# Kernel optimization log

Hardware: AMD Instinct MI355X
Metric: run time of the kernel (lower is better)

## Reference

```python
import jax, jax.numpy as jnp
import numpy as np

B, N, L = 8, 170, 336
PATCH = 16
P = L // PATCH            # 21 patches, pad_len = 0
D_MODEL = 128
D_STATE = 16
D_CONV = 4
D_INNER = 2 * D_MODEL     # expand=2
DT_RANK = 8               # ceil(d_model/16)
PRED_LEN = 96


def setup_inputs() -> dict:
    key = jax.random.key(0)
    ks = jax.random.split(key, 16)
    def nrm(k, shape, s=0.02):
        return jax.random.normal(k, shape, jnp.float32) * s
    return {
        "x": jax.random.normal(ks[0], (B, N, L), jnp.float32),
        "node_embed_map": nrm(ks[1], (1, N, 1, D_MODEL)),
        "pe_W": nrm(ks[2], (D_MODEL, PATCH), 0.1),
        "pe_b": jnp.zeros((D_MODEL,), jnp.float32),
        "pos_emb": nrm(ks[3], (1, 1, P, D_MODEL)),
        "r_W1": nrm(ks[4], (D_MODEL // 4, 3), 0.3),
        "r_b1": jnp.zeros((D_MODEL // 4,), jnp.float32),
        "r_W2": nrm(ks[5], (D_MODEL, D_MODEL // 4), 0.1),
        "r_b2": jnp.zeros((D_MODEL,), jnp.float32),
        "ln_g": jnp.ones((D_MODEL,), jnp.float32),
        "ln_b": jnp.zeros((D_MODEL,), jnp.float32),
        "in_proj_W": nrm(ks[6], (2 * D_INNER, D_MODEL), 0.05),
        "conv_W": nrm(ks[7], (D_INNER, D_CONV), 0.2),
        "conv_b": jnp.zeros((D_INNER,), jnp.float32),
        "x_proj_W": nrm(ks[8], (DT_RANK + 2 * D_STATE, D_INNER), 0.05),
        "dt_proj_W": nrm(ks[9], (D_INNER, DT_RANK), 0.3),
        "dt_proj_b": nrm(ks[10], (D_INNER,), 0.5),
        "A_log": jnp.log(jnp.broadcast_to(jnp.arange(1.0, D_STATE + 1.0, dtype=jnp.float32), (D_INNER, D_STATE))),
        "D_skip": jnp.ones((D_INNER,), jnp.float32),
        "out_proj_W": nrm(ks[11], (D_MODEL, D_INNER), 0.05),
        "head_W": nrm(ks[12], (PRED_LEN, P * D_MODEL), 0.02),
        "head_b": jnp.zeros((PRED_LEN,), jnp.float32),
    }


def _layernorm(x, g, b, eps=1e-5):
    mu = x.mean(-1, keepdims=True)
    var = ((x - mu) ** 2).mean(-1, keepdims=True)
    return (x - mu) * jax.lax.rsqrt(var + eps) * g + b


def _router(x_patch, r_W1, r_b1, r_W2, r_b2):
    # FFT energy over each length-16 patch -> low/mid/high band features -> tiny MLP gate
    X = jnp.fft.rfft(x_patch, axis=-1)          # [M, P, 9]
    energy = X.real ** 2 + X.imag ** 2
    fl = energy.shape[-1]
    s1, s2 = fl // 3, 2 * fl // 3
    feats = jnp.stack([energy[..., :s1].sum(-1),
                       energy[..., s1:s2].sum(-1),
                       energy[..., s2:].sum(-1)], axis=-1)
    feats = feats / (feats.sum(-1, keepdims=True) + 1e-6)
    h = jax.nn.relu(feats @ r_W1.T + r_b1)
    return jax.nn.sigmoid(h @ r_W2.T + r_b2)    # [M, P, d_model]


def _mamba(u, in_proj_W, conv_W, conv_b, x_proj_W, dt_proj_W, dt_proj_b, A_log, D_skip, out_proj_W):
    # u: [M, T, d_model]  (Mamba block: in_proj -> causal dwconv -> SSM scan -> gate -> out_proj)
    M, T, _ = u.shape
    xz = u @ in_proj_W.T                        # [M, T, 2*d_inner]
    xc, z = jnp.split(xz, 2, axis=-1)
    # causal depthwise conv1d, kernel D_CONV
    xp = jnp.pad(xc, ((0, 0), (D_CONV - 1, 0), (0, 0)))
    conv = conv_b + sum(xp[:, k:k + T, :] * conv_W[:, k] for k in range(D_CONV))
    xs = jax.nn.silu(conv)                      # [M, T, d_inner]
    proj = xs @ x_proj_W.T                      # [M, T, dt_rank + 2*d_state]
    dt_in = proj[..., :DT_RANK]
    Bm = proj[..., DT_RANK:DT_RANK + D_STATE]
    Cm = proj[..., DT_RANK + D_STATE:]
    dt = jax.nn.softplus(dt_in @ dt_proj_W.T + dt_proj_b)  # [M, T, d_inner]
    A = -jnp.exp(A_log)                         # [d_inner, d_state]

    def step(h, inp):
        dt_t, B_t, C_t, u_t = inp               # [M,d_inner], [M,d_state], [M,d_state], [M,d_inner]
        dA = jnp.exp(dt_t[..., None] * A)       # [M, d_inner, d_state]
        h = dA * h + (dt_t * u_t)[..., None] * B_t[:, None, :]
        y = jnp.einsum('mds,ms->md', h, C_t)
        return h, y

    h0 = jnp.zeros((M, D_INNER, D_STATE), jnp.float32)
    _, ys = jax.lax.scan(step, h0, (jnp.moveaxis(dt, 1, 0), jnp.moveaxis(Bm, 1, 0),
                                    jnp.moveaxis(Cm, 1, 0), jnp.moveaxis(xs, 1, 0)))
    y = jnp.moveaxis(ys, 0, 1) + xs * D_skip
    y = y * jax.nn.silu(z)
    return y @ out_proj_W.T


def reference(x, node_embed_map, pe_W, pe_b, pos_emb, r_W1, r_b1, r_W2, r_b2,
              ln_g, ln_b, in_proj_W, conv_W, conv_b, x_proj_W, dt_proj_W, dt_proj_b,
              A_log, D_skip, out_proj_W, head_W, head_b):
    Bb, Nn, _ = x.shape
    x_patches = x.reshape(Bb, Nn, P, PATCH)                     # pad_len == 0 for L=336
    x_enc = x_patches @ pe_W.T + pe_b + pos_emb + node_embed_map
    x_enc_flat = x_enc.reshape(Bb * Nn, P, D_MODEL)
    gate = _router(x_patches.reshape(Bb * Nn, P, PATCH), r_W1, r_b1, r_W2, r_b2)
    x_gated = _layernorm(x_enc_flat, ln_g, ln_b) * gate
    y = _mamba(x_gated, in_proj_W, conv_W, conv_b, x_proj_W, dt_proj_W, dt_proj_b,
               A_log, D_skip, out_proj_W)
    out = (y + x_enc_flat).reshape(Bb, Nn, P * D_MODEL)         # dropout is identity (eval)
    return out @ head_W.T + head_b                              # [B, N, pred_len]
```

## Files before the change

### kernel.cpp

```cpp
#include <hip/hip_runtime.h>
#include <math.h>

#define B_ 8
#define N_ 170
#define L_ 336
#define PATCH_ 16
#define P_ 21
#define DM_ 128
#define DS_ 16
#define DI_ 256
#define PL_ 96
#define M_ (B_ * N_)
#define T_ 21
#define R_ (M_ * T_)
#define KF_ (P_ * DM_)

#define XST 260
#define ZST 256
#define UST2 130
#define EST 128

typedef __attribute__((ext_vector_type(8))) short short8;
typedef __attribute__((ext_vector_type(4))) float f32x4;
typedef __attribute__((ext_vector_type(2))) float f32x2;

__device__ inline unsigned short f2b(float f) {
    unsigned int u = __builtin_bit_cast(unsigned int, f);
    u += 0x7fff + ((u >> 16) & 1);
    return (unsigned short)(u >> 16);
}
__device__ inline float b2f(unsigned short h) {
    unsigned int u = ((unsigned int)h) << 16;
    return __builtin_bit_cast(float, u);
}
__device__ inline float fast_sigmoid(float v) {
    return __builtin_amdgcn_rcpf(1.f + __expf(-v));
}
__device__ inline f32x2 pk_fma(f32x2 a, f32x2 b, f32x2 c) {
    f32x2 d;
    asm("v_pk_fma_f32 %0, %1, %2, %3" : "=v"(d) : "v"(a), "v"(b), "v"(c));
    return d;
}
__device__ inline f32x2 pk_mul(f32x2 a, f32x2 b) {
    f32x2 d;
    asm("v_pk_mul_f32 %0, %1, %2" : "=v"(d) : "v"(a), "v"(b));
    return d;
}
__device__ inline f32x2 pk_add(f32x2 a, f32x2 b) {
    f32x2 d;
    asm("v_pk_add_f32 %0, %1, %2" : "=v"(d) : "v"(a), "v"(b));
    return d;
}
__device__ inline unsigned int cvt_pk_bf16(float a, float b) {
    unsigned int d;
    asm("v_cvt_pk_bf16_f32 %0, %1, %2" : "=v"(d) : "v"(a), "v"(b));
    return d;
}

__global__ __launch_bounds__(256) void k_convert(
    const float* __restrict__ inW, const float* __restrict__ xpW,
    const float* __restrict__ outW, const float* __restrict__ hW,
    const float* __restrict__ peW, const float* __restrict__ rW2,
    unsigned short* __restrict__ winb, unsigned short* __restrict__ wxpb,
    unsigned short* __restrict__ woutb, unsigned short* __restrict__ whb,
    unsigned short* __restrict__ peWb, unsigned short* __restrict__ rW2b)
{
    const int base = (blockIdx.x * 256 + threadIdx.x) * 2;
#pragma unroll
    for (int u = 0; u < 2; ++u) {
        int i = base + u;
        if (i < 65536) { winb[i] = f2b(inW[i]); continue; }
        i -= 65536;
        if (i < 16384) {
            int j = i >> 8;
            wxpb[i] = (j < 40) ? f2b(xpW[j * 256 + (i & 255)]) : (unsigned short)0;
            continue;
        }
        i -= 16384;
        if (i < 32768) { woutb[i] = f2b(outW[i]); continue; }
        i -= 32768;
        if (i < 258048) { whb[i] = f2b(hW[i]); continue; }
        i -= 258048;
        if (i < 4096) {
            int r = i >> 5, j = i & 31;
            peWb[i] = (j < 16) ? f2b(peW[r * 16 + j]) : (unsigned short)0;
            continue;
        }
        i -= 4096;
        if (i < 4096) { rW2b[i] = f2b(rW2[i]); }
    }
}

__global__ __launch_bounds__(256, 4) void k_fused(
    const float* __restrict__ x, const float* __restrict__ nem,
    const unsigned short* __restrict__ peWb, const float* __restrict__ peB,
    const float* __restrict__ posE,
    const float* __restrict__ rW1, const float* __restrict__ rB1,
    const unsigned short* __restrict__ rW2b, const float* __restrict__ rB2,
    const float* __restrict__ lnG, const float* __restrict__ lnB,
    const unsigned short* __restrict__ winb,
    const float* __restrict__ convW, const float* __restrict__ convB,
    const unsigned short* __restrict__ wxpb,
    const float* __restrict__ dtW, const float* __restrict__ dtB,
    const float* __restrict__ Dsk,
    const unsigned short* __restrict__ woutb,
    unsigned short* __restrict__ feat)
{
    __shared__ __align__(16) char lds[27136];
    unsigned short* xss   = (unsigned short*)(lds + 0);
    unsigned short* zsl   = (unsigned short*)(lds + 10920);
    unsigned short* usj   = (unsigned short*)(lds + 21672);
    float*          pjs   = (float*)(lds + 21680);
    unsigned short* gs    = (unsigned short*)(lds + 0);
    unsigned short* pa    = (unsigned short*)(lds + 8192);
    float*          es    = (float*)(lds + 10920);
    float*          ctst  = (float*)(lds + 11680);
    float*          pn    = (float*)(lds + 11808);
    unsigned short* xencs = (unsigned short*)(lds + 12320);
    unsigned short* ha    = (unsigned short*)(lds + 21680);

    const int m = blockIdx.x;
    const int n = m % N_;
    const int tid = threadIdx.x;
    const int lane = tid & 63;
    const int w = tid >> 6;
    const int lo = lane & 15, kq = (lane >> 4) * 8;
    const int rl = (lane >> 4) * 4, cl = lane & 15;

    unsigned int resp[2][2][2];

    if (tid < 84) {
        const float4 f = *(const float4*)(x + m * L_ + tid * 4);
        const int p = tid >> 2, jj = (tid & 3) * 4;
        unsigned int u0 = cvt_pk_bf16(f.x, f.y);
        unsigned int u1 = cvt_pk_bf16(f.z, f.w);
        *(uint2*)&pa[p * 40 + jj] = make_uint2(u0, u1);
    }
    for (int i = tid; i < 384; i += 256) {
        const int p = i / 12, q = i - p * 12;
        *(unsigned int*)&pa[p * 40 + 16 + q * 2] = 0u;
    }
    if (tid < 88) {
        const int p = 21 + tid / 8, q = tid & 7;
        *(unsigned int*)&pa[p * 40 + q * 2] = 0u;
    }
    if (tid < 16) {
        float s, c;
        sincosf((float)tid * (6.283185307179586f / 16.f), &s, &c);
        ctst[tid] = c; ctst[16 + tid] = s;
    }
    if (tid >= 64 && tid < 192) pn[tid - 64] = peB[tid - 64] + nem[n * DM_ + tid - 64];
    __syncthreads();

    if (tid < P_ * 9) {
        const int i = tid;
        const int p = i / 9, bin = i - p * 9;
        short8 xv0 = *(const short8*)&pa[p * 40];
        short8 xv1 = *(const short8*)&pa[p * 40 + 8];
        float re = 0.f, im = 0.f;
#pragma unroll
        for (int j = 0; j < PATCH_; ++j) {
            int idx = (bin * j) & 15;
            float xv = b2f((unsigned short)((j < 8) ? xv0[j] : xv1[j - 8]));
            re = fmaf(xv, ctst[idx], re);
            im = fmaf(xv, -ctst[16 + idx], im);
        }
        es[i] = re * re + im * im;
    }
    {
        const unsigned short* bb = peWb + (w * 32 + lo) * 32 + kq;
        short8 b0 = *(const short8*)bb;
        short8 b1 = *(const short8*)(bb + 16 * 32);
        short8 a0 = *(const short8*)&pa[lo * 40 + kq];
        short8 a1 = *(const short8*)&pa[(16 + lo) * 40 + kq];
        f32x4 z = {0.f, 0.f, 0.f, 0.f};
        f32x4 C[2][2];
        C[0][0] = __builtin_amdgcn_mfma_f32_16x16x32_bf16(a0, b0, z, 0, 0, 0);
        C[0][1] = __builtin_amdgcn_mfma_f32_16x16x32_bf16(a0, b1, z, 0, 0, 0);
        C[1][0] = __builtin_amdgcn_mfma_f32_16x16x32_bf16(a1, b0, z, 0, 0, 0);
        C[1][1] = __builtin_amdgcn_mfma_f32_16x16x32_bf16(a1, b1, z, 0, 0, 0);
#pragma unroll
        for (int mi = 0; mi < 2; ++mi)
#pragma unroll
            for (int ni = 0; ni < 2; ++ni) {
                const int col = w * 32 + ni * 16 + cl;
                const float pncol = pn[col];
                const int row0 = mi * 16 + rl;
                const int rc0 = (row0 + 0 < P_) ? row0 + 0 : P_ - 1;
                const int rc1 = (row0 + 1 < P_) ? row0 + 1 : P_ - 1;
                const int rc2 = (row0 + 2 < P_) ? row0 + 2 : P_ - 1;
                const int rc3 = (row0 + 3 < P_) ? row0 + 3 : P_ - 1;
                float v0 = C[mi][ni][0] + pncol + posE[rc0 * DM_ + col];
                float v1 = C[mi][ni][1] + pncol + posE[rc1 * DM_ + col];
                float v2 = C[mi][ni][2] + pncol + posE[rc2 * DM_ + col];
                float v3 = C[mi][ni][3] + pncol + posE[rc3 * DM_ + col];
                const unsigned int p0 = cvt_pk_bf16(v0, v1);
                const unsigned int p1 = cvt_pk_bf16(v2, v3);
                resp[mi][ni][0] = p0;
                resp[mi][ni][1] = p1;
                xencs[(row0 + 0) * EST + col] = (unsigned short)p0;
                xencs[(row0 + 1) * EST + col] = (unsigned short)(p0 >> 16);
                xencs[(row0 + 2) * EST + col] = (unsigned short)p1;
                xencs[(row0 + 3) * EST + col] = (unsigned short)(p1 >> 16);
            }
    }
    __syncthreads();

    for (int idx = tid; idx < P_ * 32; idx += 256) {
        const int p = idx >> 5, i = idx & 31;
        const float* e = &es[p * 9];
        float b0 = e[0] + e[1] + e[2];
        float b1 = e[3] + e[4] + e[5];
        float b2 = e[6] + e[7] + e[8];
        float inv = __builtin_amdgcn_rcpf(b0 + b1 + b2 + 1e-6f);
        float hv = rB1[i];
        hv = fmaf(b0 * inv, rW1[i * 3 + 0], hv);
        hv = fmaf(b1 * inv, rW1[i * 3 + 1], hv);
        hv = fmaf(b2 * inv, rW1[i * 3 + 2], hv);
        ha[p * 40 + i] = f2b(hv > 0.f ? hv : 0.f);
    }
    __syncthreads();

    {
        const unsigned short* bb = rW2b + (w * 32 + lo) * 32 + kq;
        short8 b0 = *(const short8*)bb;
        short8 b1 = *(const short8*)(bb + 16 * 32);
        short8 a0 = *(const short8*)&ha[lo * 40 + kq];
        short8 a1 = *(const short8*)&ha[(16 + lo) * 40 + kq];
        f32x4 z = {0.f, 0.f, 0.f, 0.f};
        f32x4 C[2][2];
        C[0][0] = __builtin_amdgcn_mfma_f32_16x16x32_bf16(a0, b0, z, 0, 0, 0);
        C[0][1] = __builtin_amdgcn_mfma_f32_16x16x32_bf16(a0, b1, z, 0, 0, 0);
        C[1][0] = __builtin_amdgcn_mfma_f32_16x16x32_bf16(a1, b0, z, 0, 0, 0);
        C[1][1] = __builtin_amdgcn_mfma_f32_16x16x32_bf16(a1, b1, z, 0, 0, 0);
#pragma unroll
        for (int mi = 0; mi < 2; ++mi)
#pragma unroll
            for (int ni = 0; ni < 2; ++ni) {
                const int col = w * 32 + ni * 16 + cl;
                const float rb = rB2[col];
                float s0 = fast_sigmoid(C[mi][ni][0] + rb);
                float s1 = fast_sigmoid(C[mi][ni][1] + rb);
                float s2 = fast_sigmoid(C[mi][ni][2] + rb);
                float s3 = fast_sigmoid(C[mi][ni][3] + rb);
                const unsigned int p0 = cvt_pk_bf16(s0, s1);
                const unsigned int p1 = cvt_pk_bf16(s2, s3);
                const int row0 = mi * 16 + rl;
                gs[(row0 + 0) * EST + col] = (unsigned short)p0;
                gs[(row0 + 1) * EST + col] = (unsigned short)(p0 >> 16);
                gs[(row0 + 2) * EST + col] = (unsigned short)p1;
                gs[(row0 + 3) * EST + col] = (unsigned short)(p1 >> 16);
            }
    }
    __syncthreads();

    {
        const float lg0 = lnG[lane], lg1 = lnG[lane + 64];
        const float lb0 = lnB[lane], lb1 = lnB[lane + 64];
        for (int it = 0; it < 6; ++it) {
            const int p = it * 4 + w;
            if (p >= P_) continue;
            float xe0 = b2f(xencs[p * EST + lane]);
            float xe1 = b2f(xencs[p * EST + 64 + lane]);
            float g0 = b2f(gs[p * EST + lane]);
            float g1 = b2f(gs[p * EST + 64 + lane]);
            float s = xe0 + xe1, s2 = xe0 * xe0 + xe1 * xe1;
#pragma unroll
            for (int off = 32; off; off >>= 1) {
                s += __shfl_xor(s, off);
                s2 += __shfl_xor(s2, off);
            }
            float mu = s * (1.f / 128.f);
            float var = s2 * (1.f / 128.f) - mu * mu;
            float rs = rsqrtf(var + 1e-5f);
            float u0 = ((xe0 - mu) * rs * lg0 + lb0) * g0;
            float u1 = ((xe1 - mu) * rs * lg1 + lb1) * g1;
            const unsigned int pk = cvt_pk_bf16(u0, u1);
            usj[p * UST2 + lane]      = (unsigned short)pk;
            usj[p * UST2 + 64 + lane] = (unsigned short)(pk >> 16);
        }
    }
    __syncthreads();

    {
        const int rA1 = (16 + lo > P_ - 1) ? (P_ - 1) : (16 + lo);
#pragma unroll 1
        for (int pp = 0; pp < 4; ++pp) {
            f32x4 C[2][2];
#pragma unroll
            for (int mi = 0; mi < 2; ++mi)
#pragma unroll
                for (int ni = 0; ni < 2; ++ni) C[mi][ni] = (f32x4){0.f, 0.f, 0.f, 0.f};

            const unsigned short* bbase = winb + (size_t)(w * 128 + pp * 32 + lo) * DM_ + kq;
            __builtin_amdgcn_s_setprio(1);
#pragma unroll
            for (int k0 = 0; k0 < DM_; k0 += 32) {
                short8 a0 = *(const short8*)&usj[lo * UST2 + k0 + kq];
                short8 a1 = *(const short8*)&usj[rA1 * UST2 + k0 + kq];
#pragma unroll
                for (int ni = 0; ni < 2; ++ni) {
                    short8 b = *(const short8*)(bbase + ni * 16 * DM_ + k0);
                    C[0][ni] = __builtin_amdgcn_mfma_f32_16x16x32_bf16(a0, b, C[0][ni], 0, 0, 0);
                    C[1][ni] = __builtin_amdgcn_mfma_f32_16x16x32_bf16(a1, b, C[1][ni], 0, 0, 0);
                }
            }
            __builtin_amdgcn_s_setprio(0);
            const int cb0 = (w & 1) * 128 + pp * 32 + cl;
            if (w < 2) {
#pragma unroll
                for (int ni = 0; ni < 2; ++ni) {
                    const int col = cb0 + ni * 16;
#pragma unroll
                    for (int mi = 0; mi < 2; ++mi) {
                        const unsigned int p0 = cvt_pk_bf16(C[mi][ni][0], C[mi][ni][1]);
                        const unsigned int p1 = cvt_pk_bf16(C[mi][ni][2], C[mi][ni][3]);
                        const int row0 = mi * 16 + rl;
                        if (row0 + 0 < T_) xss[(row0 + 0) * XST + col] = (unsigned short)p0;
                        if (row0 + 1 < T_) xss[(row0 + 1) * XST + col] = (unsigned short)(p0 >> 16);
                        if (row0 + 2 < T_) xss[(row0 + 2) * XST + col] = (unsigned short)p1;
                        if (row0 + 3 < T_) xss[(row0 + 3) * XST + col] = (unsigned short)(p1 >> 16);
                    }
                }
            } else {
#pragma unroll
                for (int ni = 0; ni < 2; ++ni) {
                    const int col = cb0 + ni * 16;
#pragma unroll
                    for (int mi = 0; mi < 2; ++mi) {
                        float v0 = C[mi][ni][0]; v0 = v0 * fast_sigmoid(v0);
                        float v1 = C[mi][ni][1]; v1 = v1 * fast_sigmoid(v1);
                        float v2 = C[mi][ni][2]; v2 = v2 * fast_sigmoid(v2);
                        float v3 = C[mi][ni][3]; v3 = v3 * fast_sigmoid(v3);
                        const unsigned int p0 = cvt_pk_bf16(v0, v1);
                        const unsigned int p1 = cvt_pk_bf16(v2, v3);
                        const int row0 = mi * 16 + rl;
                        if (row0 + 0 < T_) zsl[(row0 + 0) * ZST + col] = (unsigned short)p0;
                        if (row0 + 1 < T_) zsl[(row0 + 1) * ZST + col] = (unsigned short)(p0 >> 16);
                        if (row0 + 2 < T_) zsl[(row0 + 2) * ZST + col] = (unsigned short)p1;
                        if (row0 + 3 < T_) zsl[(row0 + 3) * ZST + col] = (unsigned short)(p1 >> 16);
                    }
                }
            }
        }
    }
    __syncthreads();

    {
        const int d = tid;
        float4 cw = *(const float4*)(convW + d * 4);
        const float cb = convB[d];
        float c[T_];
#pragma unroll
        for (int t = 0; t < T_; ++t) c[t] = b2f(xss[t * XST + d]);
        float v[T_];
#pragma unroll
        for (int t = 0; t < T_; ++t) {
            float a0 = (t >= 3) ? c[t - 3] : 0.f;
            float a1 = (t >= 2) ? c[t - 2] : 0.f;
            float a2 = (t >= 1) ? c[t - 1] : 0.f;
            float vv = cb;
            vv = fmaf(a0, cw.x, vv);
            vv = fmaf(a1, cw.y, vv);
            vv = fmaf(a2, cw.z, vv);
            vv = fmaf(c[t], cw.w, vv);
            v[t] = vv * fast_sigmoid(vv);
        }
#pragma unroll
        for (int tp = 0; tp < 10; ++tp) {
            const unsigned int pk = cvt_pk_bf16(v[tp * 2], v[tp * 2 + 1]);
            xss[(tp * 2 + 0) * XST + d] = (unsigned short)pk;
            xss[(tp * 2 + 1) * XST + d] = (unsigned short)(pk >> 16);
        }
        xss[20 * XST + d] = (unsigned short)cvt_pk_bf16(v[20], v[20]);
    }
    __syncthreads();

    {
        const int mt = w >> 1, nt = w & 1;
        const unsigned short* ar = &xss[(mt * 16 + lo) * XST + kq];
        const unsigned short* bp0 = wxpb + (nt * 32 + lo) * DI_ + kq;
        const unsigned short* bp1 = bp0 + 16 * DI_;
        f32x4 c0 = {0.f, 0.f, 0.f, 0.f}, c1 = c0;
        __builtin_amdgcn_s_setprio(1);
#pragma unroll
        for (int k0 = 0; k0 < DI_; k0 += 32) {
            short8 a  = *(const short8*)(ar + k0);
            short8 b0 = *(const short8*)(bp0 + k0);
            short8 b1 = *(const short8*)(bp1 + k0);
            c0 = __builtin_amdgcn_mfma_f32_16x16x32_bf16(a, b0, c0, 0, 0, 0);
            c1 = __builtin_amdgcn_mfma_f32_16x16x32_bf16(a, b1, c1, 0, 0, 0);
        }
        __builtin_amdgcn_s_setprio(0);
#pragma unroll
        for (int r = 0; r < 4; ++r) {
            const int row = mt * 16 + rl + r;
            const int ca = nt * 32 + cl, cb = ca + 16;
            if (row < T_) {
                if (ca < 40) pjs[row * 40 + ca] = c0[r];
                if (cb < 40) pjs[row * 40 + cb] = c1[r];
            }
        }
    }
    __syncthreads();

    {
        const int d = tid;
        f32x2 dw2[4];
        {
            const f32x2* dtW2 = (const f32x2*)(dtW + d * 8);
#pragma unroll
            for (int q = 0; q < 4; ++q) dw2[q] = dtW2[q];
        }
        const float db = dtB[d], Dv = Dsk[d];
        const f32x4* pj4 = (const f32x4*)pjs;
        f32x2 h2[8];
#pragma unroll
        for (int q = 0; q < 8; ++q) h2[q] = (f32x2){0.f, 0.f};
        float ypend = 0.f;
#pragma unroll
        for (int t = 0; t < T_; ++t) {
            f32x4 d0 = pj4[t * 10 + 0];
            f32x4 d1 = pj4[t * 10 + 1];
            f32x2 acc = {db, 0.f};
            acc = pk_fma(__builtin_shufflevector(d0, d0, 0, 1), dw2[0], acc);
            acc = pk_fma(__builtin_shufflevector(d0, d0, 2, 3), dw2[1], acc);
            acc = pk_fma(__builtin_shufflevector(d1, d1, 0, 1), dw2[2], acc);
            acc = pk_fma(__builtin_shufflevector(d1, d1, 2, 3), dw2[3], acc);
            float a = acc.x + acc.y;
            float qe = __expf(a);
            float dt = (a > 20.f) ? a : __logf(1.f + qe);
            float e1 = __builtin_amdgcn_rcpf(1.f + qe);
            float e2 = e1 * e1;
            float ut = b2f(xss[t * XST + d]);
            float zq = b2f(zsl[t * ZST + d]);
            float wk = dt * ut;
            f32x2 wk2 = {wk, wk};
            f32x2 e22 = {e2, e2};
            f32x2 dA2 = {e1, e2};
            f32x2 y2 = {0.f, 0.f};
#pragma unroll
            for (int q2 = 0; q2 < 4; ++q2) {
                f32x4 B4 = pj4[t * 10 + 2 + q2];
                f32x4 C4 = pj4[t * 10 + 6 + q2];
#pragma unroll
                for (int hh = 0; hh < 2; ++hh) {
                    const int q = 2 * q2 + hh;
                    f32x2 Bq = hh ? __builtin_shufflevector(B4, B4, 2, 3)
                                  : __builtin_shufflevector(B4, B4, 0, 1);
                    f32x2 Cq = hh ? __builtin_shufflevector(C4, C4, 2, 3)
                                  : __builtin_shufflevector(C4, C4, 0, 1);
                    if (q) dA2 = pk_mul(dA2, e22);
                    h2[q] = pk_fma(dA2, h2[q], pk_mul(wk2, Bq));
                    y2 = pk_fma(h2[q], Cq, y2);
                }
            }
            float yv = fmaf(ut, Dv, y2.x + y2.y) * zq;
            if (t & 1) {
                const unsigned int pk = cvt_pk_bf16(ypend, yv);
                xss[(t - 1) * XST + d] = (unsigned short)pk;
                xss[t * XST + d]       = (unsigned short)(pk >> 16);
            } else {
                ypend = yv;
            }
        }
        xss[20 * XST + d] = (unsigned short)cvt_pk_bf16(ypend, ypend);
    }
    __syncthreads();

    {
        f32x4 C[2][2];
#pragma unroll
        for (int mi = 0; mi < 2; ++mi)
#pragma unroll
            for (int ni = 0; ni < 2; ++ni) C[mi][ni] = (f32x4){0.f, 0.f, 0.f, 0.f};

        const unsigned short* bbase = woutb + (size_t)(w * 32 + lo) * DI_ + kq;
        __builtin_amdgcn_s_setprio(1);
#pragma unroll
        for (int k0 = 0; k0 < DI_; k0 += 32) {
            short8 a0 = *(const short8*)&xss[lo * XST + k0 + kq];
            short8 a1 = *(const short8*)&xss[(16 + lo) * XST + k0 + kq];
#pragma unroll
            for (int ni = 0; ni < 2; ++ni) {
                short8 b = *(const short8*)(bbase + ni * 16 * DI_ + k0);
                C[0][ni] = __builtin_amdgcn_mfma_f32_16x16x32_bf16(a0, b, C[0][ni], 0, 0, 0);
                C[1][ni] = __builtin_amdgcn_mfma_f32_16x16x32_bf16(a1, b, C[1][ni], 0, 0, 0);
            }
        }
        __builtin_amdgcn_s_setprio(0);
        unsigned short* fb = feat + (size_t)m * T_ * DM_;
#pragma unroll
        for (int mi = 0; mi < 2; ++mi)
#pragma unroll
            for (int ni = 0; ni < 2; ++ni) {
                const int col = w * 32 + ni * 16 + cl;
                const unsigned int pr0 = resp[mi][ni][0];
                const unsigned int pr1 = resp[mi][ni][1];
                f32x2 r01, r23;
                r01.x = __builtin_bit_cast(float, pr0 << 16);
                r01.y = __builtin_bit_cast(float, pr0 & 0xffff0000u);
                r23.x = __builtin_bit_cast(float, pr1 << 16);
                r23.y = __builtin_bit_cast(float, pr1 & 0xffff0000u);
                f32x2 c01 = {C[mi][ni][0], C[mi][ni][1]};
                f32x2 c23 = {C[mi][ni][2], C[mi][ni][3]};
                f32x2 s01 = pk_add(c01, r01);
                f32x2 s23 = pk_add(c23, r23);
                const unsigned int q0 = cvt_pk_bf16(s01.x, s01.y);
                const unsigned int q1 = cvt_pk_bf16(s23.x, s23.y);
                const int row0 = mi * 16 + rl;
                if (row0 + 0 < T_) fb[(row0 + 0) * DM_ + col] = (unsigned short)q0;
                if (row0 + 1 < T_) fb[(row0 + 1) * DM_ + col] = (unsigned short)(q0 >> 16);
                if (row0 + 2 < T_) fb[(row0 + 2) * DM_ + col] = (unsigned short)q1;
                if (row0 + 3 < T_) fb[(row0 + 3) * DM_ + col] = (unsigned short)(q1 >> 16);
            }
    }
}

__global__ __launch_bounds__(512) void k_gemm_head(
    const unsigned short* __restrict__ feat, const unsigned short* __restrict__ W,
    const float* __restrict__ hB, float* __restrict__ out)
{
    __shared__ float red[8 * 512];
    const int bid = blockIdx.x;
    const int wm = bid / 3, wn = bid % 3;
    const int tid = threadIdx.x, w = tid >> 6, lane = tid & 63;
    const int r0 = wm * 16, n0 = wn * 32;
    const int lo = lane & 15, kq = (lane >> 4) * 8;
    const unsigned short* ap  = feat + (size_t)(r0 + lo) * KF_ + kq;
    const unsigned short* bp0 = W + (size_t)(n0 + lo) * KF_ + kq;
    const unsigned short* bp1 = bp0 + 16 * KF_;
    f32x4 c0 = {0.f, 0.f, 0.f, 0.f}, c1 = c0;
    for (int s = w; s < 84; s += 8) {
        const int k0 = s * 32;
        short8 a  = *(const short8*)(ap + k0);
        short8 b0 = *(const short8*)(bp0 + k0);
        short8 b1 = *(const short8*)(bp1 + k0);
        c0 = __builtin_amdgcn_mfma_f32_16x16x32_bf16(a, b0, c0, 0, 0, 0);
        c1 = __builtin_amdgcn_mfma_f32_16x16x32_bf16(a, b1, c1, 0, 0, 0);
    }
    float* rw = &red[w * 512 + lane * 8];
#pragma unroll
    for (int r = 0; r < 4; ++r) { rw[r] = c0[r]; rw[4 + r] = c1[r]; }
    __syncthreads();

    {
        const int f = tid;
        float s = red[f] + red[512 + f] + red[1024 + f] + red[1536 + f]
                + red[2048 + f] + red[2560 + f] + red[3072 + f] + red[3584 + f];
        const int l = f >> 3, v = f & 7;
        const int row = r0 + ((l >> 4) << 2) + (v & 3);
        const int col = n0 + (l & 15) + ((v >= 4) ? 16 : 0);
        out[row * PL_ + col] = s + hB[col];
    }
}

extern "C" void kernel_launch(void* const* d_in, const int* in_sizes, int n_in,
                              void* d_out, int out_size, void* d_ws, size_t ws_size,
                              hipStream_t stream)
{
    const float* x     = (const float*)d_in[0];
    const float* nem   = (const float*)d_in[1];
    const float* peW   = (const float*)d_in[2];
    const float* peB   = (const float*)d_in[3];
    const float* posE  = (const float*)d_in[4];
    const float* rW1   = (const float*)d_in[5];
    const float* rB1   = (const float*)d_in[6];
    const float* rW2   = (const float*)d_in[7];
    const float* rB2   = (const float*)d_in[8];
    const float* lnG   = (const float*)d_in[9];
    const float* lnB   = (const float*)d_in[10];
    const float* inW   = (const float*)d_in[11];
    const float* convW = (const float*)d_in[12];
    const float* convB = (const float*)d_in[13];
    const float* xpW   = (const float*)d_in[14];
    const float* dtW   = (const float*)d_in[15];
    const float* dtB   = (const float*)d_in[16];
    const float* Dsk   = (const float*)d_in[18];
    const float* outW  = (const float*)d_in[19];
    const float* hW    = (const float*)d_in[20];
    const float* hB    = (const float*)d_in[21];
    float* out = (float*)d_out;

    char* ws = (char*)d_ws;
    size_t off = 0;
    auto alloc = [&](size_t bytes) { size_t o = off; off = (off + bytes + 255) & ~(size_t)255; return o; };
    unsigned short* feat  = (unsigned short*)(ws + alloc((size_t)R_ * DM_ * 2));
    unsigned short* winb  = (unsigned short*)(ws + alloc(512 * 128 * 2));
    unsigned short* wxpb  = (unsigned short*)(ws + alloc(64 * 256 * 2));
    unsigned short* woutb = (unsigned short*)(ws + alloc(128 * 256 * 2));
    unsigned short* whb   = (unsigned short*)(ws + alloc(96 * KF_ * 2));
    unsigned short* peWb  = (unsigned short*)(ws + alloc(128 * 32 * 2));
    unsigned short* rW2b  = (unsigned short*)(ws + alloc(128 * 32 * 2));

    k_convert<<<744, 256, 0, stream>>>(inW, xpW, outW, hW, peW, rW2,
                                       winb, wxpb, woutb, whb, peWb, rW2b);
    k_fused<<<M_, 256, 0, stream>>>(x, nem, peWb, peB, posE,
                                    rW1, rB1, rW2b, rB2, lnG, lnB,
                                    winb, convW, convB, wxpb,
                                    dtW, dtB, Dsk, woutb, feat);
    k_gemm_head<<<255, 512, 0, stream>>>(feat, whb, hB, out);
}
```

Baseline: 182.2 us.

## Fuse head projection into fused Mamba kernel, removing feature round-trip

The separate head GEMM kernel is removed. Each fused block now keeps its 21x128 bf16 feature tile in LDS and computes the 96 outputs with scalar FMAs over a transposed, pair-packed head weight produced in the convert kernel. This drops the global write and re-read of the feature tensor and one kernel launch. In exchange, every block streams the full head weight (about 516 KB) through cache using non-MFMA scalar math on only 192 threads, which could cost more than it saves.

```diff
diff --git a/kernel.cpp b/kernel.cpp
--- a/kernel.cpp
+++ b/kernel.cpp
@@ -33,6 +33,12 @@
     unsigned int u = ((unsigned int)h) << 16;
     return __builtin_bit_cast(float, u);
 }
+__device__ inline float b2f_lo(unsigned int u) {
+    return __builtin_bit_cast(float, u << 16);
+}
+__device__ inline float b2f_hi(unsigned int u) {
+    return __builtin_bit_cast(float, u & 0xffff0000u);
+}
 __device__ inline float fast_sigmoid(float v) {
     return __builtin_amdgcn_rcpf(1.f + __expf(-v));
 }
@@ -62,7 +68,7 @@
     const float* __restrict__ outW, const float* __restrict__ hW,
     const float* __restrict__ peW, const float* __restrict__ rW2,
     unsigned short* __restrict__ winb, unsigned short* __restrict__ wxpb,
-    unsigned short* __restrict__ woutb, unsigned short* __restrict__ whb,
+    unsigned short* __restrict__ woutb, unsigned short* __restrict__ whbT,
     unsigned short* __restrict__ peWb, unsigned short* __restrict__ rW2b)
 {
     const int base = (blockIdx.x * 256 + threadIdx.x) * 2;
@@ -79,7 +85,12 @@
         i -= 16384;
         if (i < 32768) { woutb[i] = f2b(outW[i]); continue; }
         i -= 32768;
-        if (i < 258048) { whb[i] = f2b(hW[i]); continue; }
+        if (i < 258048) {
+            const int k2 = i / 192, r = i - k2 * 192;
+            const int c = r >> 1, p = r & 1;
+            whbT[i] = f2b(hW[c * KF_ + 2 * k2 + p]);
+            continue;
+        }
         i -= 258048;
         if (i < 4096) {
             int r = i >> 5, j = i & 31;
@@ -104,7 +115,8 @@
     const float* __restrict__ dtW, const float* __restrict__ dtB,
     const float* __restrict__ Dsk,
     const unsigned short* __restrict__ woutb,
-    unsigned short* __restrict__ feat)
+    const unsigned short* __restrict__ whbT, const float* __restrict__ hB,
+    float* __restrict__ out)
 {
     __shared__ __align__(16) char lds[27136];
     unsigned short* xss   = (unsigned short*)(lds + 0);
@@ -118,6 +130,8 @@
     float*          pn    = (float*)(lds + 11808);
     unsigned short* xencs = (unsigned short*)(lds + 12320);
     unsigned short* ha    = (unsigned short*)(lds + 21680);
+    unsigned short* fls   = (unsigned short*)(lds + 21680);
+    float*          redh  = (float*)(lds + 0);
 
     const int m = blockIdx.x;
     const int n = m % N_;
@@ -489,7 +503,6 @@
             }
         }
         __builtin_amdgcn_s_setprio(0);
-        unsigned short* fb = feat + (size_t)m * T_ * DM_;
 #pragma unroll
         for (int mi = 0; mi < 2; ++mi)
 #pragma unroll
@@ -509,49 +522,32 @@
                 const unsigned int q0 = cvt_pk_bf16(s01.x, s01.y);
                 const unsigned int q1 = cvt_pk_bf16(s23.x, s23.y);
                 const int row0 = mi * 16 + rl;
-                if (row0 + 0 < T_) fb[(row0 + 0) * DM_ + col] = (unsigned short)q0;
-                if (row0 + 1 < T_) fb[(row0 + 1) * DM_ + col] = (unsigned short)(q0 >> 16);
-                if (row0 + 2 < T_) fb[(row0 + 2) * DM_ + col] = (unsigned short)q1;
-                if (row0 + 3 < T_) fb[(row0 + 3) * DM_ + col] = (unsigned short)(q1 >> 16);
-            }
-    }
-}
-
-__global__ __launch_bounds__(512) void k_gemm_head(
-    const unsigned short* __restrict__ feat, const unsigned short* __restrict__ W,
-    const float* __restrict__ hB, float* __restrict__ out)
-{
-    __shared__ float red[8 * 512];
-    const int bid = blockIdx.x;
-    const int wm = bid / 3, wn = bid % 3;
-    const int tid = threadIdx.x, w = tid >> 6, lane = tid & 63;
-    const int r0 = wm * 16, n0 = wn * 32;
-    const int lo = lane & 15, kq = (lane >> 4) * 8;
-    const unsigned short* ap  = feat + (size_t)(r0 + lo) * KF_ + kq;
-    const unsigned short* bp0 = W + (size_t)(n0 + lo) * KF_ + kq;
-    const unsigned short* bp1 = bp0 + 16 * KF_;
-    f32x4 c0 = {0.f, 0.f, 0.f, 0.f}, c1 = c0;
-    for (int s = w; s < 84; s += 8) {
-        const int k0 = s * 32;
-        short8 a  = *(const short8*)(ap + k0);
-        short8 b0 = *(const short8*)(bp0 + k0);
-        short8 b1 = *(const short8*)(bp1 + k0);
-        c0 = __builtin_amdgcn_mfma_f32_16x16x32_bf16(a, b0, c0, 0, 0, 0);
-        c1 = __builtin_amdgcn_mfma_f32_16x16x32_bf16(a, b1, c1, 0, 0, 0);
-    }
-    float* rw = &red[w * 512 + lane * 8];
-#pragma unroll
-    for (int r = 0; r < 4; ++r) { rw[r] = c0[r]; rw[4 + r] = c1[r]; }
-    __syncthreads();
-
-    {
-        const int f = tid;
-        float s = red[f] + red[512 + f] + red[1024 + f] + red[1536 + f]
-                + red[2048 + f] + red[2560 + f] + red[3072 + f] + red[3584 + f];
-        const int l = f >> 3, v = f & 7;
-        const int row = r0 + ((l >> 4) << 2) + (v & 3);
-        const int col = n0 + (l & 15) + ((v >= 4) ? 16 : 0);
-        out[row * PL_ + col] = s + hB[col];
+                if (row0 + 0 < T_) fls[(row0 + 0) * DM_ + col] = (unsigned short)q0;
+                if (row0 + 1 < T_) fls[(row0 + 1) * DM_ + col] = (unsigned short)(q0 >> 16);
+                if (row0 + 2 < T_) fls[(row0 + 2) * DM_ + col] = (unsigned short)q1;
+                if (row0 + 3 < T_) fls[(row0 + 3) * DM_ + col] = (unsigned short)(q1 >> 16);
+            }
+    }
+    __syncthreads();
+
+    if (tid < 192) {
+        const int h = (tid >= 96) ? 1 : 0;
+        const int c = tid - h * 96;
+        const unsigned int* fp = (const unsigned int*)fls + h * 672;
+        const unsigned int* wq = (const unsigned int*)whbT + (size_t)(h * 672) * 96 + c;
+        float acc = 0.f;
+#pragma unroll 4
+        for (int k2 = 0; k2 < 672; ++k2) {
+            const unsigned int f = fp[k2];
+            const unsigned int ww = wq[(size_t)k2 * 96];
+            acc = fmaf(b2f_lo(f), b2f_lo(ww), acc);
+            acc = fmaf(b2f_hi(f), b2f_hi(ww), acc);
+        }
+        redh[tid] = acc;
+    }
+    __syncthreads();
+    if (tid < PL_) {
+        out[(size_t)m * PL_ + tid] = redh[tid] + redh[PL_ + tid] + hB[tid];
     }
 }
 
@@ -585,19 +581,18 @@
     char* ws = (char*)d_ws;
     size_t off = 0;
     auto alloc = [&](size_t bytes) { size_t o = off; off = (off + bytes + 255) & ~(size_t)255; return o; };
-    unsigned short* feat  = (unsigned short*)(ws + alloc((size_t)R_ * DM_ * 2));
     unsigned short* winb  = (unsigned short*)(ws + alloc(512 * 128 * 2));
     unsigned short* wxpb  = (unsigned short*)(ws + alloc(64 * 256 * 2));
     unsigned short* woutb = (unsigned short*)(ws + alloc(128 * 256 * 2));
-    unsigned short* whb   = (unsigned short*)(ws + alloc(96 * KF_ * 2));
+    unsigned short* whbT  = (unsigned short*)(ws + alloc(96 * KF_ * 2));
     unsigned short* peWb  = (unsigned short*)(ws + alloc(128 * 32 * 2));
     unsigned short* rW2b  = (unsigned short*)(ws + alloc(128 * 32 * 2));
 
     k_convert<<<744, 256, 0, stream>>>(inW, xpW, outW, hW, peW, rW2,
-                                       winb, wxpb, woutb, whb, peWb, rW2b);
+                                       winb, wxpb, woutb, whbT, peWb, rW2b);
     k_fused<<<M_, 256, 0, stream>>>(x, nem, peWb, peB, posE,
                                     rW1, rB1, rW2b, rB2, lnG, lnB,
                                     winb, convW, convB, wxpb,
-                                    dtW, dtB, Dsk, woutb, feat);
-    k_gemm_head<<<255, 512, 0, stream>>>(feat, whb, hB, out);
-}
+                                    dtW, dtB, Dsk, woutb,
+                                    whbT, hB, out);
+}
```

Result: slower. 235.7 us (+29.4%).
